# Optimization experiments

Hardware: AMD Instinct MI355X
Metric: run time of the kernel (lower is better)

The kernel has to match this reference:

```python
import jax, jax.numpy as jnp
import numpy as np

B, N, FDIM = 8, 2048, 256
ASSIGN_RATIO = 0.1
K = int(N * ASSIGN_RATIO) + 1  # num coarse nodes per graph (205)
DENSITY = 0.01


def setup_inputs() -> dict:
    key = jax.random.key(0)
    k1, k2, k3 = jax.random.split(key, 3)
    x = jax.random.normal(k1, (B, N, FDIM), dtype=jnp.float32)
    u = jax.random.uniform(k2, (B, N, N), dtype=jnp.float32)
    adj = jnp.where(u < DENSITY, u, 0.0)
    adj = 0.5 * (adj + jnp.swapaxes(adj, 1, 2))  # symmetric weighted adjacency
    W = jax.random.normal(k3, (FDIM, 1), dtype=jnp.float32) * 0.05
    b = jnp.zeros((1,), dtype=jnp.float32)
    return {"x": x, "adj": adj, "W": W, "b": b}


def _coarsen(x, adj, W, b):
    I = jnp.eye(N, dtype=adj.dtype)
    # --- GCNConv attention score (self-loops + symmetric normalization) ---
    A_hat = adj + I                       # [B,N,N]
    dg = A_hat.sum(-1) ** -0.5            # deg >= 1 via self-loop
    gcn_norm = dg[:, :, None] * A_hat * dg[:, None, :]
    alpha = jnp.einsum('bnm,bmf,fo->bno', gcn_norm, x, W) + b
    alpha = jax.nn.sigmoid(alpha ** 2)[..., 0]   # [B,N], sigmoid(gcn^2)
    # --- normalize_batch_adj: D^{-1/2}(A+I)D^{-1/2}, zero isolated rows ---
    d = jnp.clip(A_hat.sum(-1), 1.0, None) ** -0.5
    norm_adj = d[:, :, None] * A_hat * d[:, None, :]
    norm_adj = norm_adj * (adj.sum(-1) > 0).astype(adj.dtype)[:, :, None]
    # --- top-k cut on attention ---
    topv, topi = jax.lax.top_k(alpha, K)  # [B,K]
    cut = topv[:, K - 1]                  # k-th largest value per graph
    cut_alpha = jax.nn.relu(alpha + 1e-7 - cut[:, None])   # [B,N]
    # --- assignment matrix S = L1-row-normalized(norm_adj * cut_alpha_cols) ---
    S = norm_adj * cut_alpha[:, None, :]
    S = S / jnp.clip(jnp.abs(S).sum(-1, keepdims=True), 1e-12, None)
    # --- coarsening matmuls ---
    x_c = jnp.einsum('bnm,bnf->bmf', S, x)                 # S^T x
    coarse = jnp.einsum('bnm,bnk,bkl->bml', S, adj, S)     # S^T A S
    coarse = jnp.floor(coarse * 1e4) / 1e4                 # 4-digit truncation
    return x_c, coarse, S, topi


def reference(x, adj, W, b):
    return _coarsen(x, adj, W, b)
```

## Files before the change

### kernel.cpp

```cpp
#include <hip/hip_runtime.h>
#include <cstdint>
#include <cstddef>

#define BB 8
#define NN 2048
#define FD 256
#define KK 205
#define CAP 96
#define SELCAP 256

__global__ __launch_bounds__(256) void k_y(const float* __restrict__ x, const float* __restrict__ W,
                                           float* __restrict__ y) {
  int lane = threadIdx.x & 63, wv = threadIdx.x >> 6;
  int row = blockIdx.x * 4 + wv;
  const float* xr = x + (size_t)row * FD;
  float s = xr[lane] * W[lane] + xr[lane + 64] * W[lane + 64]
          + xr[lane + 128] * W[lane + 128] + xr[lane + 192] * W[lane + 192];
#pragma unroll
  for (int off = 32; off > 0; off >>= 1) s += __shfl_down(s, off);
  if (lane == 0) y[row] = s;
}

__global__ __launch_bounds__(256) void k_sparsify(const float* __restrict__ adj, int* __restrict__ ell_idx,
                                                  float* __restrict__ ell_val, int* __restrict__ ell_cnt,
                                                  float* __restrict__ dg, float* __restrict__ rowsum) {
  int r = blockIdx.x;
  const float* arow = adj + (size_t)r * NN;
  int t = threadIdx.x;
  float lv[8]; int li[8]; int lc = 0; float ls = 0.f;
#pragma unroll
  for (int j = 0; j < 8; ++j) {
    int m = t + j * 256;
    float v = arow[m];
    if (v != 0.f) { lv[lc] = v; li[lc] = m; ++lc; ls += v; }
  }
  __shared__ int cnts[256];
  __shared__ float ssum[256];
  cnts[t] = lc; ssum[t] = ls;
  __syncthreads();
  for (int off = 1; off < 256; off <<= 1) {
    int add = (t >= off) ? cnts[t - off] : 0;
    __syncthreads();
    cnts[t] += add;
    __syncthreads();
  }
  int start = cnts[t] - lc;
  size_t base = (size_t)r * CAP;
  for (int e = 0; e < lc; ++e) {
    int p = start + e;
    if (p < CAP) { ell_idx[base + p] = li[e]; ell_val[base + p] = lv[e]; }
  }
  for (int off = 128; off > 0; off >>= 1) {
    if (t < off) ssum[t] += ssum[t + off];
    __syncthreads();
  }
  if (t == 0) {
    int tot = cnts[255]; if (tot > CAP) tot = CAP;
    ell_cnt[r] = tot;
    float rs = ssum[0];
    rowsum[r] = rs;
    dg[r] = 1.0f / sqrtf(1.0f + rs);
  }
}

__global__ __launch_bounds__(256) void k_alpha(const int* __restrict__ ell_idx, const float* __restrict__ ell_val,
                                               const int* __restrict__ ell_cnt, const float* __restrict__ dg,
                                               const float* __restrict__ y, const float* __restrict__ bptr,
                                               float* __restrict__ alpha) {
  int lane = threadIdx.x & 63, wv = threadIdx.x >> 6;
  int r = blockIdx.x * 4 + wv;
  int b = r / NN;
  int cnt = ell_cnt[r];
  size_t base = (size_t)r * CAP;
  const float* dgb = dg + (size_t)b * NN;
  const float* yb = y + (size_t)b * NN;
  float acc = 0.f;
  for (int j = lane; j < cnt; j += 64) {
    int m = ell_idx[base + j];
    acc += ell_val[base + j] * dgb[m] * yb[m];
  }
#pragma unroll
  for (int off = 32; off > 0; off >>= 1) acc += __shfl_down(acc, off);
  if (lane == 0) {
    float dgn = dg[r];
    float z = dgn * (acc + dgn * y[r]) + bptr[0];
    float t2 = z * z;
    alpha[r] = 1.0f / (1.0f + expf(-t2));
  }
}

__global__ __launch_bounds__(1024) void k_topk(const float* __restrict__ alpha, float* __restrict__ cutv,
                                               float* __restrict__ out_topi) {
  __shared__ unsigned long long keys[NN];
  int b = blockIdx.x, t = threadIdx.x;
  for (int i = t; i < NN; i += 1024) {
    unsigned int ab = __float_as_uint(alpha[(size_t)b * NN + i]);
    keys[i] = ((unsigned long long)ab << 32) | (unsigned int)(NN - 1 - i);
  }
  __syncthreads();
  for (int k2 = 2; k2 <= NN; k2 <<= 1) {
    for (int j = k2 >> 1; j > 0; j >>= 1) {
      for (int i = t; i < NN; i += 1024) {
        int ixj = i ^ j;
        if (ixj > i) {
          unsigned long long a = keys[i], c = keys[ixj];
          bool desc = ((i & k2) == 0);
          bool sw = desc ? (a < c) : (a > c);
          if (sw) { keys[i] = c; keys[ixj] = a; }
        }
      }
      __syncthreads();
    }
  }
  if (t < KK) {
    unsigned int low = (unsigned int)(keys[t] & 0xffffffffULL);
    out_topi[(size_t)b * KK + t] = (float)(NN - 1 - (int)low);
  }
  if (t == 0) cutv[b] = __uint_as_float((unsigned int)(keys[KK - 1] >> 32));
}

__global__ __launch_bounds__(256) void k_selcut(const float* __restrict__ alpha, const float* __restrict__ cutv,
                                                float* __restrict__ cutA, int* __restrict__ selidx,
                                                int* __restrict__ sel_list, int* __restrict__ sel_cnt) {
  int r = blockIdx.x * 256 + threadIdx.x;
  int b = r / NN, n = r % NN;
  float ca = fmaxf(alpha[r] + 1e-7f - cutv[b], 0.0f);
  cutA[r] = ca;
  int s = -1;
  if (ca > 0.f) {
    s = atomicAdd(&sel_cnt[b], 1);
    if (s < SELCAP) sel_list[b * SELCAP + s] = n; else s = -1;
  }
  selidx[r] = s;
}

__global__ __launch_bounds__(256) void k_sbuild(const int* __restrict__ ell_idx, const float* __restrict__ ell_val,
                                                const int* __restrict__ ell_cnt, const float* __restrict__ dg,
                                                const float* __restrict__ rowsum, const float* __restrict__ cutA,
                                                const int* __restrict__ selidx, float* __restrict__ inv_eff,
                                                float* __restrict__ Sc, float* __restrict__ outS) {
  __shared__ float row[NN];
  __shared__ float scrow[SELCAP];
  __shared__ int   sidx[CAP];
  __shared__ float sterm[CAP];
  __shared__ float red[256];
  __shared__ float s_inv, s_dv;
  int r = blockIdx.x;
  int b = r >> 11;
  int t = threadIdx.x;
#pragma unroll
  for (int j = 0; j < NN / 256; ++j) row[t + j * 256] = 0.f;
  if (t < SELCAP) scrow[t] = 0.f;
  int cnt = ell_cnt[r];
  size_t base = (size_t)r * CAP;
  float dgn = dg[r];
  const float* dgb = dg + (size_t)b * NN;
  const float* cab = cutA + (size_t)b * NN;
  const int* sib = selidx + (size_t)b * NN;
  float part = 0.f;
  for (int j = t; j < cnt; j += 256) {
    int m = ell_idx[base + j];
    float term = dgn * ell_val[base + j] * dgb[m] * cab[m];
    sidx[j] = m; sterm[j] = term;
    part += term;
  }
  red[t] = part;
  __syncthreads();
  for (int off = 128; off > 0; off >>= 1) {
    if (t < off) red[t] += red[t + off];
    __syncthreads();
  }
  if (t == 0) {
    float diag = dgn * dgn * cutA[r];
    float rho = red[0] + diag;
    float inv = (rowsum[r] > 0.f) ? (1.0f / fmaxf(rho, 1e-12f)) : 0.f;
    s_inv = inv; s_dv = diag * inv;
    inv_eff[r] = inv;
  }
  __syncthreads();
  float inv = s_inv;
  for (int j = t; j < cnt; j += 256) {
    float v = sterm[j] * inv;
    row[sidx[j]] = v;
    int si = sib[sidx[j]];
    if (si >= 0) scrow[si] = v;
  }
  __syncthreads();
  if (t == 0) {
    int n = r & (NN - 1);
    row[n] += s_dv;
    int si = sib[n];
    if (si >= 0) scrow[si] += s_dv;
  }
  __syncthreads();
  float4* dst = (float4*)(outS + (size_t)r * NN);
  const float4* src = (const float4*)row;
#pragma unroll
  for (int j = 0; j < NN / 4 / 256; ++j) dst[t + j * 256] = src[t + j * 256];
  if (t < SELCAP) Sc[(size_t)r * SELCAP + t] = scrow[t];
}

__global__ __launch_bounds__(256) void k_xc(const float* __restrict__ x, const int* __restrict__ ell_idx,
                                            const float* __restrict__ ell_val, const int* __restrict__ ell_cnt,
                                            const float* __restrict__ dg, const float* __restrict__ cutA,
                                            const float* __restrict__ inv_eff, const int* __restrict__ sel_list,
                                            const int* __restrict__ sel_cnt, float* __restrict__ xc) {
  int b = blockIdx.x & 7;
  int i = blockIdx.x >> 3;
  int nsel = sel_cnt[b]; if (nsel > SELCAP) nsel = SELCAP;
  if (i >= nsel) return;
  int m = sel_list[b * SELCAP + i];
  int rm = b * NN + m;
  int cnt = ell_cnt[rm];
  size_t base = (size_t)rm * CAP;
  __shared__ int cn[CAP + 1];
  __shared__ float cw[CAP + 1];
  float dgm = dg[rm], cam = cutA[rm];
  for (int j = threadIdx.x; j <= cnt; j += 256) {
    if (j < cnt) {
      int n = ell_idx[base + j];
      cn[j] = n;
      cw[j] = ell_val[base + j] * dg[b * NN + n] * dgm * cam * inv_eff[b * NN + n];
    } else {
      cn[j] = m;
      cw[j] = dgm * dgm * cam * inv_eff[rm];
    }
  }
  __syncthreads();
  int f = threadIdx.x;
  float acc = 0.f;
  for (int e = 0; e <= cnt; ++e) acc += cw[e] * x[((size_t)(b * NN + cn[e])) * FD + f];
  xc[(size_t)rm * FD + f] = acc;
}

__global__ __launch_bounds__(256) void k_M(const int* __restrict__ ell_idx, const float* __restrict__ ell_val,
                                           const int* __restrict__ ell_cnt, const float* __restrict__ Sc,
                                           float* __restrict__ Mmat) {
  int b = blockIdx.x & 7;
  int n = blockIdx.x >> 3;
  int r = b * NN + n;
  int t = threadIdx.x;
  __shared__ int srk[CAP];
  __shared__ float sav[CAP];
  int cnt = ell_cnt[r];
  size_t base = (size_t)r * CAP;
  for (int e = t; e < cnt; e += 256) {
    srk[e] = b * NN + ell_idx[base + e];
    sav[e] = ell_val[base + e];
  }
  __syncthreads();
  float a0 = 0.f;
  for (int e = 0; e < cnt; ++e) a0 += sav[e] * Sc[(size_t)srk[e] * SELCAP + t];
  Mmat[(size_t)r * SELCAP + t] = a0;
}

__global__ __launch_bounds__(256) void k_coarse2(const int* __restrict__ ell_idx, const float* __restrict__ ell_val,
                                                 const int* __restrict__ ell_cnt, const float* __restrict__ dg,
                                                 const float* __restrict__ cutA, const float* __restrict__ inv_eff,
                                                 const int* __restrict__ sel_list, const int* __restrict__ sel_cnt,
                                                 const float* __restrict__ Mmat, float* __restrict__ coarse) {
  int b = blockIdx.x & 7;
  int i = blockIdx.x >> 3;
  int nsel = sel_cnt[b]; if (nsel > SELCAP) nsel = SELCAP;
  if (i >= nsel) return;
  int m = sel_list[b * SELCAP + i];
  int rm = b * NN + m;
  int cnt = ell_cnt[rm];
  size_t base = (size_t)rm * CAP;
  __shared__ int cn[CAP + 1];
  __shared__ float cw[CAP + 1];
  float dgm = dg[rm], cam = cutA[rm];
  for (int j = threadIdx.x; j <= cnt; j += 256) {
    if (j < cnt) {
      int n = ell_idx[base + j];
      cn[j] = b * NN + n;
      cw[j] = ell_val[base + j] * dg[b * NN + n] * dgm * cam * inv_eff[b * NN + n];
    } else {
      cn[j] = rm;
      cw[j] = dgm * dgm * cam * inv_eff[rm];
    }
  }
  __syncthreads();
  int t = threadIdx.x;
  float a0 = 0.f;
  for (int e = 0; e <= cnt; ++e) {
    float w = cw[e];
    if (w == 0.f) continue;
    a0 += w * Mmat[(size_t)cn[e] * SELCAP + t];
  }
  if (t < nsel) {
    float* crow = coarse + (size_t)rm * NN;
    crow[sel_list[b * SELCAP + t]] = floorf(a0 * 10000.0f) / 10000.0f;
  }
}

extern "C" void kernel_launch(void* const* d_in, const int* in_sizes, int n_in,
                              void* d_out, int out_size, void* d_ws, size_t ws_size,
                              hipStream_t stream) {
  (void)in_sizes; (void)n_in; (void)ws_size; (void)out_size;
  const float* x = (const float*)d_in[0];
  const float* adj = (const float*)d_in[1];
  const float* W = (const float*)d_in[2];
  const float* bptr = (const float*)d_in[3];

  float* out = (float*)d_out;
  const size_t XC_SZ = (size_t)BB * NN * FD;
  const size_t CO_SZ = (size_t)BB * NN * NN;
  const size_t S_SZ  = (size_t)BB * NN * NN;
  float* out_xc = out;
  float* out_co = out + XC_SZ;
  float* out_S  = out + XC_SZ + CO_SZ;
  float* out_ti = out + XC_SZ + CO_SZ + S_SZ;

  char* w = (char*)d_ws;
  int*   ell_idx = (int*)w;   w += (size_t)BB * NN * CAP * 4;
  float* ell_val = (float*)w; w += (size_t)BB * NN * CAP * 4;
  float* Sc      = (float*)w; w += (size_t)BB * NN * SELCAP * 4;
  float* Mmat    = (float*)w; w += (size_t)BB * NN * SELCAP * 4;
  int*   ell_cnt = (int*)w;   w += (size_t)BB * NN * 4;
  float* dg      = (float*)w; w += (size_t)BB * NN * 4;
  float* rowsum  = (float*)w; w += (size_t)BB * NN * 4;
  float* yv      = (float*)w; w += (size_t)BB * NN * 4;
  float* alpha   = (float*)w; w += (size_t)BB * NN * 4;
  float* cutA    = (float*)w; w += (size_t)BB * NN * 4;
  float* inv_eff = (float*)w; w += (size_t)BB * NN * 4;
  int*   selidx  = (int*)w;   w += (size_t)BB * NN * 4;
  float* cutv    = (float*)w; w += (size_t)BB * 4;
  int*   sel_cnt = (int*)w;   w += (size_t)BB * 4;
  int*   sel_list= (int*)w;   w += (size_t)BB * SELCAP * 4;

  hipMemsetAsync(out, 0, (XC_SZ + CO_SZ) * sizeof(float), stream);
  hipMemsetAsync(sel_cnt, 0, BB * sizeof(int), stream);

  k_y<<<BB * NN / 4, 256, 0, stream>>>(x, W, yv);
  k_sparsify<<<BB * NN, 256, 0, stream>>>(adj, ell_idx, ell_val, ell_cnt, dg, rowsum);
  k_alpha<<<BB * NN / 4, 256, 0, stream>>>(ell_idx, ell_val, ell_cnt, dg, yv, bptr, alpha);
  k_topk<<<BB, 1024, 0, stream>>>(alpha, cutv, out_ti);
  k_selcut<<<BB * NN / 256, 256, 0, stream>>>(alpha, cutv, cutA, selidx, sel_list, sel_cnt);
  k_sbuild<<<BB * NN, 256, 0, stream>>>(ell_idx, ell_val, ell_cnt, dg, rowsum, cutA, selidx,
                                        inv_eff, Sc, out_S);
  k_xc<<<BB * SELCAP, 256, 0, stream>>>(x, ell_idx, ell_val, ell_cnt, dg, cutA, inv_eff,
                                        sel_list, sel_cnt, out_xc);
  k_M<<<BB * NN, 256, 0, stream>>>(ell_idx, ell_val, ell_cnt, Sc, Mmat);
  k_coarse2<<<BB * SELCAP, 256, 0, stream>>>(ell_idx, ell_val, ell_cnt, dg, cutA, inv_eff,
                                             sel_list, sel_cnt, Mmat, out_co);
}
```

Baseline: 555.6 us.

## Fuse y into sparsify, replace bitonic top-k with rank count, merge xc/coarse epilogue

Folds the x·W projection into the adjacency sparsify kernel and merges the x_c and coarse epilogue kernels, which share the same weight setup, into one. The single-block-per-graph bitonic sort is replaced by a parallel rank-counting kernel over 64 blocks that writes top-k indices and the cut value directly and resets sel_cnt, which removes a memset. The aim is fewer launches and a shorter serial top-k stage. The rank kernel does O(N^2) comparisons per graph, but they run in parallel from shared memory.

```diff
diff --git a/kernel.cpp b/kernel.cpp
--- a/kernel.cpp
+++ b/kernel.cpp
@@ -9,21 +9,11 @@
 #define CAP 96
 #define SELCAP 256
 
-__global__ __launch_bounds__(256) void k_y(const float* __restrict__ x, const float* __restrict__ W,
-                                           float* __restrict__ y) {
-  int lane = threadIdx.x & 63, wv = threadIdx.x >> 6;
-  int row = blockIdx.x * 4 + wv;
-  const float* xr = x + (size_t)row * FD;
-  float s = xr[lane] * W[lane] + xr[lane + 64] * W[lane + 64]
-          + xr[lane + 128] * W[lane + 128] + xr[lane + 192] * W[lane + 192];
-#pragma unroll
-  for (int off = 32; off > 0; off >>= 1) s += __shfl_down(s, off);
-  if (lane == 0) y[row] = s;
-}
-
-__global__ __launch_bounds__(256) void k_sparsify(const float* __restrict__ adj, int* __restrict__ ell_idx,
-                                                  float* __restrict__ ell_val, int* __restrict__ ell_cnt,
-                                                  float* __restrict__ dg, float* __restrict__ rowsum) {
+__global__ __launch_bounds__(256) void k_spy(const float* __restrict__ adj, const float* __restrict__ x,
+                                             const float* __restrict__ W, int* __restrict__ ell_idx,
+                                             float* __restrict__ ell_val, int* __restrict__ ell_cnt,
+                                             float* __restrict__ dg, float* __restrict__ rowsum,
+                                             float* __restrict__ y) {
   int r = blockIdx.x;
   const float* arow = adj + (size_t)r * NN;
   int t = threadIdx.x;
@@ -61,6 +51,14 @@
     rowsum[r] = rs;
     dg[r] = 1.0f / sqrtf(1.0f + rs);
   }
+  __syncthreads();
+  ssum[t] = x[(size_t)r * FD + t] * W[t];
+  __syncthreads();
+  for (int off = 128; off > 0; off >>= 1) {
+    if (t < off) ssum[t] += ssum[t + off];
+    __syncthreads();
+  }
+  if (t == 0) y[r] = ssum[0];
 }
 
 __global__ __launch_bounds__(256) void k_alpha(const int* __restrict__ ell_idx, const float* __restrict__ ell_val,
@@ -89,34 +87,31 @@
   }
 }
 
-__global__ __launch_bounds__(1024) void k_topk(const float* __restrict__ alpha, float* __restrict__ cutv,
-                                               float* __restrict__ out_topi) {
-  __shared__ unsigned long long keys[NN];
-  int b = blockIdx.x, t = threadIdx.x;
-  for (int i = t; i < NN; i += 1024) {
-    unsigned int ab = __float_as_uint(alpha[(size_t)b * NN + i]);
-    keys[i] = ((unsigned long long)ab << 32) | (unsigned int)(NN - 1 - i);
-  }
-  __syncthreads();
-  for (int k2 = 2; k2 <= NN; k2 <<= 1) {
-    for (int j = k2 >> 1; j > 0; j >>= 1) {
-      for (int i = t; i < NN; i += 1024) {
-        int ixj = i ^ j;
-        if (ixj > i) {
-          unsigned long long a = keys[i], c = keys[ixj];
-          bool desc = ((i & k2) == 0);
-          bool sw = desc ? (a < c) : (a > c);
-          if (sw) { keys[i] = c; keys[ixj] = a; }
-        }
-      }
-      __syncthreads();
-    }
-  }
-  if (t < KK) {
-    unsigned int low = (unsigned int)(keys[t] & 0xffffffffULL);
-    out_topi[(size_t)b * KK + t] = (float)(NN - 1 - (int)low);
-  }
-  if (t == 0) cutv[b] = __uint_as_float((unsigned int)(keys[KK - 1] >> 32));
+__global__ __launch_bounds__(256) void k_rank(const float* __restrict__ alpha, float* __restrict__ cutv,
+                                              float* __restrict__ out_topi, int* __restrict__ sel_cnt) {
+  __shared__ unsigned int keys[NN];
+  int b = blockIdx.x & 7;
+  int chunk = blockIdx.x >> 3;
+  int t = threadIdx.x;
+  if (chunk == 0 && t == 0) sel_cnt[b] = 0;
+  const float* ab = alpha + (size_t)b * NN;
+  for (int i = t; i < NN; i += 256) keys[i] = __float_as_uint(ab[i]);
+  __syncthreads();
+  int i = chunk * 256 + t;
+  unsigned int ai = keys[i];
+  int rank = 0;
+  const uint4* k4 = (const uint4*)keys;
+#pragma unroll 4
+  for (int j4 = 0; j4 < NN / 4; ++j4) {
+    uint4 v = k4[j4];
+    int j = j4 * 4;
+    rank += (v.x > ai) || (v.x == ai && (j + 0) < i);
+    rank += (v.y > ai) || (v.y == ai && (j + 1) < i);
+    rank += (v.z > ai) || (v.z == ai && (j + 2) < i);
+    rank += (v.w > ai) || (v.w == ai && (j + 3) < i);
+  }
+  if (rank < KK) out_topi[(size_t)b * KK + rank] = (float)i;
+  if (rank == KK - 1) cutv[b] = __uint_as_float(ai);
 }
 
 __global__ __launch_bounds__(256) void k_selcut(const float* __restrict__ alpha, const float* __restrict__ cutv,
@@ -200,39 +195,6 @@
   if (t < SELCAP) Sc[(size_t)r * SELCAP + t] = scrow[t];
 }
 
-__global__ __launch_bounds__(256) void k_xc(const float* __restrict__ x, const int* __restrict__ ell_idx,
-                                            const float* __restrict__ ell_val, const int* __restrict__ ell_cnt,
-                                            const float* __restrict__ dg, const float* __restrict__ cutA,
-                                            const float* __restrict__ inv_eff, const int* __restrict__ sel_list,
-                                            const int* __restrict__ sel_cnt, float* __restrict__ xc) {
-  int b = blockIdx.x & 7;
-  int i = blockIdx.x >> 3;
-  int nsel = sel_cnt[b]; if (nsel > SELCAP) nsel = SELCAP;
-  if (i >= nsel) return;
-  int m = sel_list[b * SELCAP + i];
-  int rm = b * NN + m;
-  int cnt = ell_cnt[rm];
-  size_t base = (size_t)rm * CAP;
-  __shared__ int cn[CAP + 1];
-  __shared__ float cw[CAP + 1];
-  float dgm = dg[rm], cam = cutA[rm];
-  for (int j = threadIdx.x; j <= cnt; j += 256) {
-    if (j < cnt) {
-      int n = ell_idx[base + j];
-      cn[j] = n;
-      cw[j] = ell_val[base + j] * dg[b * NN + n] * dgm * cam * inv_eff[b * NN + n];
-    } else {
-      cn[j] = m;
-      cw[j] = dgm * dgm * cam * inv_eff[rm];
-    }
-  }
-  __syncthreads();
-  int f = threadIdx.x;
-  float acc = 0.f;
-  for (int e = 0; e <= cnt; ++e) acc += cw[e] * x[((size_t)(b * NN + cn[e])) * FD + f];
-  xc[(size_t)rm * FD + f] = acc;
-}
-
 __global__ __launch_bounds__(256) void k_M(const int* __restrict__ ell_idx, const float* __restrict__ ell_val,
                                            const int* __restrict__ ell_cnt, const float* __restrict__ Sc,
                                            float* __restrict__ Mmat) {
@@ -254,11 +216,12 @@
   Mmat[(size_t)r * SELCAP + t] = a0;
 }
 
-__global__ __launch_bounds__(256) void k_coarse2(const int* __restrict__ ell_idx, const float* __restrict__ ell_val,
-                                                 const int* __restrict__ ell_cnt, const float* __restrict__ dg,
-                                                 const float* __restrict__ cutA, const float* __restrict__ inv_eff,
-                                                 const int* __restrict__ sel_list, const int* __restrict__ sel_cnt,
-                                                 const float* __restrict__ Mmat, float* __restrict__ coarse) {
+__global__ __launch_bounds__(256) void k_epi(const float* __restrict__ x, const int* __restrict__ ell_idx,
+                                             const float* __restrict__ ell_val, const int* __restrict__ ell_cnt,
+                                             const float* __restrict__ dg, const float* __restrict__ cutA,
+                                             const float* __restrict__ inv_eff, const int* __restrict__ sel_list,
+                                             const int* __restrict__ sel_cnt, const float* __restrict__ Mmat,
+                                             float* __restrict__ xc, float* __restrict__ coarse) {
   int b = blockIdx.x & 7;
   int i = blockIdx.x >> 3;
   int nsel = sel_cnt[b]; if (nsel > SELCAP) nsel = SELCAP;
@@ -282,15 +245,18 @@
   }
   __syncthreads();
   int t = threadIdx.x;
-  float a0 = 0.f;
+  float axc = 0.f, aco = 0.f;
   for (int e = 0; e <= cnt; ++e) {
     float w = cw[e];
     if (w == 0.f) continue;
-    a0 += w * Mmat[(size_t)cn[e] * SELCAP + t];
-  }
+    size_t rn = (size_t)cn[e];
+    axc += w * x[rn * FD + t];
+    aco += w * Mmat[rn * SELCAP + t];
+  }
+  xc[(size_t)rm * FD + t] = axc;
   if (t < nsel) {
     float* crow = coarse + (size_t)rm * NN;
-    crow[sel_list[b * SELCAP + t]] = floorf(a0 * 10000.0f) / 10000.0f;
+    crow[sel_list[b * SELCAP + t]] = floorf(aco * 10000.0f) / 10000.0f;
   }
 }
 
@@ -330,18 +296,14 @@
   int*   sel_list= (int*)w;   w += (size_t)BB * SELCAP * 4;
 
   hipMemsetAsync(out, 0, (XC_SZ + CO_SZ) * sizeof(float), stream);
-  hipMemsetAsync(sel_cnt, 0, BB * sizeof(int), stream);
-
-  k_y<<<BB * NN / 4, 256, 0, stream>>>(x, W, yv);
-  k_sparsify<<<BB * NN, 256, 0, stream>>>(adj, ell_idx, ell_val, ell_cnt, dg, rowsum);
+
+  k_spy<<<BB * NN, 256, 0, stream>>>(adj, x, W, ell_idx, ell_val, ell_cnt, dg, rowsum, yv);
   k_alpha<<<BB * NN / 4, 256, 0, stream>>>(ell_idx, ell_val, ell_cnt, dg, yv, bptr, alpha);
-  k_topk<<<BB, 1024, 0, stream>>>(alpha, cutv, out_ti);
+  k_rank<<<BB * 8, 256, 0, stream>>>(alpha, cutv, out_ti, sel_cnt);
   k_selcut<<<BB * NN / 256, 256, 0, stream>>>(alpha, cutv, cutA, selidx, sel_list, sel_cnt);
   k_sbuild<<<BB * NN, 256, 0, stream>>>(ell_idx, ell_val, ell_cnt, dg, rowsum, cutA, selidx,
                                         inv_eff, Sc, out_S);
-  k_xc<<<BB * SELCAP, 256, 0, stream>>>(x, ell_idx, ell_val, ell_cnt, dg, cutA, inv_eff,
-                                        sel_list, sel_cnt, out_xc);
   k_M<<<BB * NN, 256, 0, stream>>>(ell_idx, ell_val, ell_cnt, Sc, Mmat);
-  k_coarse2<<<BB * SELCAP, 256, 0, stream>>>(ell_idx, ell_val, ell_cnt, dg, cutA, inv_eff,
-                                             sel_list, sel_cnt, Mmat, out_co);
-}
+  k_epi<<<BB * SELCAP, 256, 0, stream>>>(x, ell_idx, ell_val, ell_cnt, dg, cutA, inv_eff,
+                                         sel_list, sel_cnt, Mmat, out_xc, out_co);
+}
```

Result: slower. 573.4 us (+3.2%).
